# Kernel tuning notes

Hardware: AMD Instinct MI355X
Metric: run time of the kernel (lower is better)

The kernel has to match this reference:

```python
import jax, jax.numpy as jnp
import numpy as np

B, H, W = 4, 512, 512
DIM = 32          # AFNet output channels; last 3 are an RGB residual
HID = 128         # AFNet hidden width
C_IN = DIM - 3    # UNet input channels
C1, C2 = 64, 128  # UNet channel widths


def _conv(x, k, stride=1):
    # x: [B,C,H,W], k: [O,I,kh,kw]
    return jax.lax.conv_general_dilated(
        x, k, (stride, stride), 'SAME',
        dimension_numbers=('NCHW', 'OIHW', 'NCHW'))


def setup_inputs() -> dict:
    key = jax.random.key(0)
    ks = jax.random.split(key, 16)
    zbuf = jax.random.uniform(ks[0], (B, H, W, 1), jnp.float32, -0.5, 2.0)
    ray = jax.random.normal(ks[1], (B, H, W, 7), jnp.float32)
    # last ray channel is a divisor -> keep it bounded away from 0
    ray = ray.at[..., 6].set(jax.random.uniform(ks[2], (B, H, W), jnp.float32, 0.5, 1.5))
    gt = jax.random.uniform(ks[3], (B, H, W, 3), jnp.float32)
    s = 0.05
    return {
        'zbuf': zbuf, 'ray': ray, 'gt': gt, 'isTrain': 0,
        'af_w0': s * jax.random.normal(ks[4], (6, HID), jnp.float32),
        'af_b0': jnp.zeros((HID,), jnp.float32),
        'af_w1': s * jax.random.normal(ks[5], (HID, HID), jnp.float32),
        'af_b1': jnp.zeros((HID,), jnp.float32),
        'af_w2': s * jax.random.normal(ks[6], (HID, DIM), jnp.float32),
        'af_b2': jnp.zeros((DIM,), jnp.float32),
        'u_k1': s * jax.random.normal(ks[7], (C1, C_IN, 3, 3), jnp.float32),
        'u_k2': s * jax.random.normal(ks[8], (C2, C1, 3, 3), jnp.float32),
        'u_k3': s * jax.random.normal(ks[9], (C1, C2 + C1, 3, 3), jnp.float32),
        'u_k4': s * jax.random.normal(ks[10], (3, C1, 3, 3), jnp.float32),
    }


def reference(zbuf, ray, gt, isTrain, af_w0, af_b0, af_w1, af_b1, af_w2, af_b2,
              u_k1, u_k2, u_k3, u_k4):
    # Eval path (isTrain == 0): no pad / random-crop.
    pix_mask = zbuf[..., 0] > 0.0                       # [B,H,W]
    dirs = ray[..., 3:6]
    # xyz_near = origin + dir * z / ray[:, -1:]  (the gathered math, done densely)
    xyz_near = ray[..., :3] + dirs * zbuf / ray[..., 6:7]
    # AFNet: pointwise MLP on (xyz_near, dir)
    fin = jnp.concatenate([xyz_near, dirs], axis=-1)    # [B,H,W,6]
    h = jax.nn.relu(jnp.einsum('bhwi,io->bhwo', fin, af_w0) + af_b0)
    h = jax.nn.relu(jnp.einsum('bhwi,io->bhwo', h, af_w1) + af_b1)
    feat = jnp.einsum('bhwi,io->bhwo', h, af_w2) + af_b2  # [B,H,W,DIM]
    # scatter: feature_map = ones; feature_map[pix_mask] = feat
    fmap = jnp.where(pix_mask[..., None], feat, jnp.float32(1.0))
    x = jnp.transpose(fmap[..., :C_IN], (0, 3, 1, 2))     # [B,C_IN,H,W]
    rgb_res = jnp.transpose(fmap[..., C_IN:], (0, 3, 1, 2))  # [B,3,H,W]
    # UNet refine
    e1 = jax.nn.relu(_conv(x, u_k1))                      # [B,64,H,W]
    d = jax.nn.relu(_conv(e1, u_k2, stride=2))            # [B,128,H/2,W/2]
    u = jnp.repeat(jnp.repeat(d, 2, axis=2), 2, axis=3)   # nearest upsample
    m = jax.nn.relu(_conv(jnp.concatenate([u, e1], axis=1), u_k3))
    img = _conv(m, u_k4) + rgb_res                        # [B,3,H,W]
    return img
```

## Files before the change

### kernel.cpp

```cpp
#include <hip/hip_runtime.h>
#include <hip/hip_bf16.h>
#include <stdint.h>

typedef __hip_bfloat16 bf16;
typedef __attribute__((ext_vector_type(8))) short short8;
typedef __attribute__((ext_vector_type(4))) float f32x4;
typedef __attribute__((ext_vector_type(16))) float f32x16;
typedef __attribute__((ext_vector_type(8))) _Float16 half8;

__device__ __forceinline__ float bf2f(bf16 x){ return __bfloat162float(x); }
__device__ __forceinline__ bf16  f2bf(float x){ return __float2bfloat16(x); }
__device__ __forceinline__ short f2bfs(float x){ union { bf16 h; short s; } u; u.h = f2bf(x); return u.s; }
__device__ __forceinline__ float bfs2f(short s){ union { bf16 h; short t; } u; u.t = s; return bf2f(u.h); }
__device__ __forceinline__ unsigned short f2hs(float x){ union { _Float16 f; unsigned short u; } c; c.f = (_Float16)x; return c.u; }

#define WB1_R   0UL
#define WB2_R   36864UL
#define WBD_R   184320UL
#define WBE_R   446464UL
#define WB4_R   520192UL
#define WMLP_R  538624UL
#define WZERO_R 583680UL
#define W_TOTAL 587776UL
#define DT_BS   8388608UL
#define E1_BS   16777216UL
#define OUT_BS  786432UL

__global__ void prep_kernel(const float* __restrict__ uk1, const float* __restrict__ uk2,
                            const float* __restrict__ uk3, const float* __restrict__ uk4,
                            const float* __restrict__ w0, const float* __restrict__ w1,
                            const float* __restrict__ w2,
                            short* __restrict__ wb1, short* __restrict__ wb2,
                            short* __restrict__ wbD, short* __restrict__ wbE,
                            short* __restrict__ wb4,
                            unsigned short* __restrict__ wfmlp, float* __restrict__ zp){
  int gidx = blockIdx.x*256 + threadIdx.x;
  if (gidx < 18432){
    int idx = gidx;
    int j = idx & 7, lane = (idx >> 3) & 63, n = (idx >> 9) & 3, t = idx >> 11;
    int co = n*16 + (lane & 15);
    int ci = (lane >> 4)*8 + j;
    float val = (ci < 29) ? uk1[(co*29 + ci)*9 + t] : 0.f;
    wb1[idx] = f2bfs(val);
  } else if (gidx < 92160){
    int idx = gidx - 18432;
    int j    = idx & 7;
    int lane = (idx >> 3) & 63;
    int n    = (idx >> 9) & 7;
    int kt   = idx >> 12;
    int t = kt % 9, ks = kt / 9;
    int co = n*16 + (lane & 15);
    int ci = ks*32 + (lane >> 4)*8 + j;
    wb2[idx] = f2bfs(uk2[(co*64 + ci)*9 + t]);
  } else if (gidx < 223232){
    int idx = gidx - 92160;
    int j    = idx & 7;
    int lane = (idx >> 3) & 63;
    int n    = (idx >> 9) & 3;
    int kD   = (idx >> 11) & 15;
    int par  = idx >> 15;
    int pr = par >> 1, pc = par & 1;
    int jx = kD & 1, jy = (kD >> 1) & 1, ks = (kD >> 2) & 1, c = kD >> 3;
    int co = n*16 + (lane & 15);
    int ci = (c*2 + ks)*32 + (lane >> 4)*8 + j;
    int ty0, ty1, tx0, tx1;
    if (pr == 0){ ty0 = jy ? 1 : 0; ty1 = jy ? 2 : 0; }
    else        { ty0 = jy ? 2 : 0; ty1 = jy ? 2 : 1; }
    if (pc == 0){ tx0 = jx ? 1 : 0; tx1 = jx ? 2 : 0; }
    else        { tx0 = jx ? 2 : 0; tx1 = jx ? 2 : 1; }
    float val = 0.f;
    for (int ty = ty0; ty <= ty1; ++ty)
      for (int tx = tx0; tx <= tx1; ++tx)
        val += uk3[(co*192 + ci)*9 + ty*3 + tx];
    wbD[idx] = f2bfs(val);
  } else if (gidx < 260096){
    int idx = gidx - 223232;
    int j    = idx & 7;
    int lane = (idx >> 3) & 63;
    int n    = (idx >> 9) & 3;
    int chunk = idx >> 11;
    int ks2 = chunk & 1, t = chunk >> 1;
    int co = n*16 + (lane & 15);
    int ci = 128 + ks2*32 + (lane >> 4)*8 + j;
    wbE[idx] = f2bfs(uk3[(co*192 + ci)*9 + t]);
  } else if (gidx < 269312){
    int idx = gidx - 260096;
    int j = idx & 7, lane = (idx >> 3) & 63, rt = idx >> 9;
    int t = rt % 9, kc = rt / 9;
    int co = lane & 15;
    int ci = kc*32 + (lane >> 4)*8 + j;
    float val = (co < 3) ? uk4[(co*64 + ci)*9 + t] : 0.f;
    wb4[idx] = f2bfs(val);
  } else if (gidx < 291840){
    int idx = gidx - 269312;
    int j = idx & 7;
    int cl = idx >> 3;
    int lane = cl & 63;
    int chunk = cl >> 6;
    int hi5 = lane >> 5, l31 = lane & 31;
    float val;
    if (chunk < 4){
      int n = chunk;
      int k = hi5*8 + j, co = n*32 + l31;
      val = (k < 6) ? w0[k*128 + co] : 0.f;
    } else if (chunk < 36){
      int c = chunk - 4; int ks = c >> 2, n = c & 3;
      int k = ks*16 + hi5*8 + j, co = n*32 + l31;
      val = w1[k*128 + co];
    } else {
      int ks = chunk - 36;
      int k = ks*16 + hi5*8 + j, co = l31;
      val = w2[k*32 + co];
    }
    union { _Float16 f; unsigned short u; } cv; cv.f = (_Float16)val;
    wfmlp[idx] = cv.u;
  } else if (gidx < 292864){
    zp[gidx - 291840] = 0.f;
  }
}

__global__ __launch_bounds__(256,3) void mlp_mfma(
    const float* __restrict__ zbuf, const float* __restrict__ ray,
    const unsigned short* __restrict__ wf,
    bf16* __restrict__ fmap, float* __restrict__ outrgb,
    size_t fmap_bs, size_t out_bs){
  __shared__ __align__(16) unsigned short hsh[4][32][128];
  __shared__ float zsh[4][32];
  const int tid = threadIdx.x;
  const int wv = tid >> 6, lane = tid & 63, h5 = lane >> 5, l31 = lane & 31;
  const int mbase = (blockIdx.x*4 + wv)*32;
  const int bz = mbase >> 18;
  const int prel = mbase & 262143;

  const float* rp = ray + (size_t)(mbase + l31)*7;
  float z  = zbuf[mbase + l31];
  float d0 = rp[3], d1 = rp[4], d2 = rp[5];
  float inv = z / rp[6];
  half8 a1 = {};
  if (h5 == 0){
    float f[6] = { rp[0]+d0*inv, rp[1]+d1*inv, rp[2]+d2*inv, d0, d1, d2 };
    #pragma unroll
    for (int j = 0; j < 6; ++j) a1[j] = (_Float16)f[j];
    zsh[wv][l31] = z;
  }

  auto hstore = [&](int row, int col, float v){
    int g = (col >> 3) ^ (row & 7);
    hsh[wv][row][g*8 + (col & 7)] = f2hs(v);
  };
  auto hread = [&](int ks) -> half8 {
    int g = (ks*2 + h5) ^ (l31 & 7);
    return *(const half8*)&hsh[wv][l31][g*8];
  };

  f32x16 acc[4];
  #pragma unroll
  for (int n = 0; n < 4; ++n){
    half8 b = *(const half8*)&wf[(n*64 + lane)*8];
    f32x16 a = {};
    acc[n] = __builtin_amdgcn_mfma_f32_32x32x16_f16(a1, b, a, 0, 0, 0);
  }
  #pragma unroll
  for (int n = 0; n < 4; ++n)
    #pragma unroll
    for (int reg = 0; reg < 16; ++reg)
      hstore((reg&3) + 8*(reg>>2) + 4*h5, n*32 + l31, fmaxf(acc[n][reg], 0.f));

  f32x16 acc2[4];
  #pragma unroll
  for (int n = 0; n < 4; ++n) acc2[n] = (f32x16){};
  #pragma unroll
  for (int ks = 0; ks < 8; ++ks){
    half8 ah = hread(ks);
    #pragma unroll
    for (int n = 0; n < 4; ++n){
      half8 b = *(const half8*)&wf[((4 + ks*4 + n)*64 + lane)*8];
      acc2[n] = __builtin_amdgcn_mfma_f32_32x32x16_f16(ah, b, acc2[n], 0, 0, 0);
    }
  }
  #pragma unroll
  for (int n = 0; n < 4; ++n)
    #pragma unroll
    for (int reg = 0; reg < 16; ++reg)
      hstore((reg&3) + 8*(reg>>2) + 4*h5, n*32 + l31, fmaxf(acc2[n][reg], 0.f));

  f32x16 a3 = {};
  #pragma unroll
  for (int ks = 0; ks < 8; ++ks){
    half8 ah = hread(ks);
    half8 b = *(const half8*)&wf[((36 + ks)*64 + lane)*8];
    a3 = __builtin_amdgcn_mfma_f32_32x32x16_f16(ah, b, a3, 0, 0, 0);
  }

  bf16* fb = fmap + (size_t)bz*fmap_bs;
  float* ob = outrgb + (size_t)bz*out_bs;
  const int c = l31;
  #pragma unroll
  for (int g = 0; g < 4; ++g){
    const int r0 = 8*g + 4*h5;
    float vs[4];
    #pragma unroll
    for (int k = 0; k < 4; ++k){
      float zz = zsh[wv][r0 + k];
      vs[k] = (zz > 0.f) ? a3[g*4 + k] : 1.0f;
    }
    const size_t p = (size_t)(prel + r0);
    if (c < 29){
      #pragma unroll
      for (int k = 0; k < 4; ++k)
        fb[(p + k)*32 + c] = f2bf(vs[k]);
    } else {
      float4 fv = { vs[0], vs[1], vs[2], vs[3] };
      *(float4*)(&ob[((size_t)(c - 29) << 18) + p]) = fv;
      #pragma unroll
      for (int k = 0; k < 4; ++k)
        fb[(p + k)*32 + c] = f2bf(0.f);
    }
  }
}

__global__ __launch_bounds__(256,2) void conv1_mfma(
    const bf16* __restrict__ fmap32, const short8* __restrict__ wb1,
    bf16* __restrict__ e1T, const float* __restrict__ zpage,
    size_t fmap_bs, size_t e1_bs){
  __shared__ short lds[8192];
  const int tid = threadIdx.x;
  const int wv = tid >> 6, lane = tid & 63;
  const int quad = lane >> 4, l15 = lane & 15;

  const int L = blockIdx.x;
  const int cpx = gridDim.x >> 3;
  const int o = (L & 7)*cpx + (L >> 3);
  const int bx = o & 31;
  const int r2 = o >> 5;
  const int by = r2 & 63;
  const int bz = r2 >> 6;

  const bf16* fb = fmap32 + (size_t)bz*fmap_bs;
  bf16* eb = e1T + (size_t)bz*e1_bs;
  const int oy0 = by*8, ox0 = bx*16;

  for (int r = 0; r < 3; ++r){
    const int d = r*256 + tid;
    const int pairI = d >> 3, slot = d & 7;
    const int sel = slot ^ (pairI & 7);
    const int p = pairI*2 + (sel >> 2);
    const int g = sel & 3;
    const int row = p / 18, col = p - row*18;
    const int gy = oy0 - 1 + row, gx = ox0 - 1 + col;
    const bool ok = (d < 720) && ((unsigned)gy < 512u) && ((unsigned)gx < 512u);
    const void* src = ok
      ? (const void*)&fb[((size_t)((gy<<9) + gx))*32 + g*8]
      : (const void*)zpage;
    __builtin_amdgcn_global_load_lds(
      (const __attribute__((address_space(1))) void*)src,
      (__attribute__((address_space(3))) void*)&lds[d*8],
      16, 0, 0);
  }
  __syncthreads();

  f32x4 acc[2][4];
  #pragma unroll
  for (int i=0;i<2;++i)
    #pragma unroll
    for (int n=0;n<4;++n) acc[i][n] = (f32x4){0.f,0.f,0.f,0.f};

  for (int t = 0; t < 9; ++t){
    const short8* bp = wb1 + (t*4)*64 + lane;
    short8 b0 = bp[0], b1 = bp[64], b2 = bp[128], b3 = bp[192];
    const int dy = t/3, dx = t - dy*3;
    #pragma unroll
    for (int i = 0; i < 2; ++i){
      const int py = wv*2 + i + dy;
      const int px = l15 + dx;
      const int p = py*18 + px;
      const int slot = (quad + 4*(p & 1)) ^ ((p >> 1) & 7);
      short8 a = *(const short8*)&lds[((p >> 1)*8 + slot)*8];
      acc[i][0] = __builtin_amdgcn_mfma_f32_16x16x32_bf16(a, b0, acc[i][0], 0, 0, 0);
      acc[i][1] = __builtin_amdgcn_mfma_f32_16x16x32_bf16(a, b1, acc[i][1], 0, 0, 0);
      acc[i][2] = __builtin_amdgcn_mfma_f32_16x16x32_bf16(a, b2, acc[i][2], 0, 0, 0);
      acc[i][3] = __builtin_amdgcn_mfma_f32_16x16x32_bf16(a, b3, acc[i][3], 0, 0, 0);
    }
  }
  __syncthreads();

  #pragma unroll
  for (int i = 0; i < 2; ++i){
    const int rowp = wv*2 + i;
    #pragma unroll
    for (int n = 0; n < 4; ++n){
      const int gq = n*2 + (l15 >> 3);
      #pragma unroll
      for (int reg = 0; reg < 4; ++reg){
        const int px = rowp*16 + quad*4 + reg;
        const int slot = gq ^ (px & 7);
        lds[(px*8 + slot)*8 + (l15 & 7)] = f2bfs(fmaxf(acc[i][n][reg], 0.f));
      }
    }
  }
  __syncthreads();
  #pragma unroll
  for (int w = 0; w < 4; ++w){
    const int s = w*256 + tid;
    const int px = s >> 3, g8 = s & 7;
    const int slot = g8 ^ (px & 7);
    short8 v = *(const short8*)&lds[(px*8 + slot)*8];
    const int gy = oy0 + (px >> 4), gx = ox0 + (px & 15);
    *(short8*)((void*)&eb[((size_t)((gy<<9) + gx))*64 + g8*8]) = v;
  }
}

__global__ __launch_bounds__(256,2) void conv2_mfma(
    const bf16* __restrict__ e1T, const short8* __restrict__ wb2,
    bf16* __restrict__ dT, const float* __restrict__ zpage,
    size_t e1_bs, size_t dt_bs){
  __shared__ short lds[36864];
  const int tid = threadIdx.x;
  const int wv = tid >> 6, lane = tid & 63;
  const int quad = lane >> 4, l15 = lane & 15;

  const int L = blockIdx.x;
  const int cpx = gridDim.x >> 3;
  const int o = (L & 7)*cpx + (L >> 3);
  const int bx = o & 15;
  const int r2 = o >> 4;
  const int by = r2 & 31;
  const int bz = r2 >> 5;

  const bf16* eb = e1T + (size_t)bz*e1_bs;
  bf16* db = dT + (size_t)bz*dt_bs;
  const int oy0 = by*8, ox0 = bx*16;
  const int iy0 = oy0*2, ix0 = ox0*2;

  for (int r = 0; r < 18; ++r){
    const int idx = r*256 + tid;
    const int g = idx & 7, p = idx >> 3;
    const int row = p / 33, col = p - row*33;
    const int gy = iy0 + row, gx = ix0 + col;
    const int gs = g ^ ((col >> 1) & 7);
    const bool ok = (p < 561) && (gy < 512) && (gx < 512);
    const void* src = ok
      ? (const void*)&eb[((size_t)((gy<<9) + gx))*64 + gs*8]
      : (const void*)zpage;
    __builtin_amdgcn_global_load_lds(
      (const __attribute__((address_space(1))) void*)src,
      (__attribute__((address_space(3))) void*)&lds[idx*8],
      16, 0, 0);
  }
  __syncthreads();

  f32x4 acc[2][8];
  #pragma unroll
  for (int i=0;i<2;++i)
    #pragma unroll
    for (int n=0;n<8;++n) acc[i][n] = (f32x4){0.f,0.f,0.f,0.f};

  for (int ks = 0; ks < 2; ++ks){
    const int cg = ks*4 + quad;
    for (int t = 0; t < 9; ++t){
      const short8* bp = wb2 + ((ks*9 + t)*8)*64 + lane;
      short8 b0 = bp[0],   b1 = bp[64],  b2 = bp[128], b3 = bp[192];
      short8 b4 = bp[256], b5 = bp[320], b6 = bp[384], b7 = bp[448];
      const int dy = t/3, dx = t - dy*3;
      #pragma unroll
      for (int i = 0; i < 2; ++i){
        const int m = wv*2 + i;
        const int py = 2*m + dy;
        const int px = 2*l15 + dx;
        const int slot = cg ^ ((px >> 1) & 7);
        short8 a = *(const short8*)&lds[((py*33 + px)*8 + slot)*8];
        acc[i][0] = __builtin_amdgcn_mfma_f32_16x16x32_bf16(a, b0, acc[i][0], 0, 0, 0);
        acc[i][1] = __builtin_amdgcn_mfma_f32_16x16x32_bf16(a, b1, acc[i][1], 0, 0, 0);
        acc[i][2] = __builtin_amdgcn_mfma_f32_16x16x32_bf16(a, b2, acc[i][2], 0, 0, 0);
        acc[i][3] = __builtin_amdgcn_mfma_f32_16x16x32_bf16(a, b3, acc[i][3], 0, 0, 0);
        acc[i][4] = __builtin_amdgcn_mfma_f32_16x16x32_bf16(a, b4, acc[i][4], 0, 0, 0);
        acc[i][5] = __builtin_amdgcn_mfma_f32_16x16x32_bf16(a, b5, acc[i][5], 0, 0, 0);
        acc[i][6] = __builtin_amdgcn_mfma_f32_16x16x32_bf16(a, b6, acc[i][6], 0, 0, 0);
        acc[i][7] = __builtin_amdgcn_mfma_f32_16x16x32_bf16(a, b7, acc[i][7], 0, 0, 0);
      }
    }
  }
  __syncthreads();

  #pragma unroll
  for (int i = 0; i < 2; ++i){
    const int m = wv*2 + i;
    #pragma unroll
    for (int n = 0; n < 8; ++n){
      #pragma unroll
      for (int reg = 0; reg < 4; ++reg){
        const int col = quad*4 + reg;
        const int px = m*16 + col;
        const int g16 = n*2 + (l15 >> 3);
        const int slot = g16 ^ (px & 15);
        lds[(px*16 + slot)*8 + (l15 & 7)] = f2bfs(fmaxf(acc[i][n][reg], 0.f));
      }
    }
  }
  __syncthreads();
  #pragma unroll
  for (int w = 0; w < 8; ++w){
    const int s = w*256 + tid;
    const int px = s >> 4, g16 = s & 15;
    const int slot = g16 ^ (px & 15);
    short8 v = *(const short8*)&lds[(px*16 + slot)*8];
    const int gy = oy0 + (px >> 4), gx = ox0 + (px & 15);
    *(short8*)((void*)&db[((size_t)((gy<<8) + gx))*128 + g16*8]) = v;
  }
}

__global__ __launch_bounds__(256,2) void conv34_mfma(
    const bf16* __restrict__ dT, const bf16* __restrict__ e1T,
    const short8* __restrict__ wbD, const short8* __restrict__ wbE,
    const short8* __restrict__ wb4,
    float* __restrict__ out, const float* __restrict__ zpage,
    size_t dt_bs, size_t e1_bs, size_t out_bs){
  __shared__ short lds[39424];
  const int tid = threadIdx.x;
  const int wv = tid >> 6, lane = tid & 63;
  const int quad = lane >> 4, l15 = lane & 15;

  const int L = blockIdx.x;
  const int cpx = gridDim.x >> 3;
  const int o = (L & 7)*cpx + (L >> 3);
  const int bx = o % 18;
  const int rem = o / 18;
  const int by = rem & 63;
  const int bz = rem >> 6;

  const bf16* dTb = dT + (size_t)bz*dt_bs;
  const bf16* e1b = e1T + (size_t)bz*e1_bs;
  float* outb = out + (size_t)bz*out_bs;
  const int gy0 = by * 8;
  const int gx0 = bx * 30;
  const int dy0 = (gy0 >> 1) - 1;
  const int dx0 = (gx0 >> 1) - 1;
  const int rm0 = (wv >> 1) ^ 1;
  const int mx0 = (wv & 1) ^ 1;
  f32x4 acc[5][4];
  #pragma unroll
  for (int i=0;i<5;++i)
    #pragma unroll
    for (int n=0;n<4;++n) acc[i][n] = (f32x4){0.f,0.f,0.f,0.f};

  short* DB0 = lds;
  short* DB1 = lds + 6656;
  short* EB  = lds + 13312;

  auto stage_dT = [&](int c, short* db){
    #pragma unroll
    for (int r = 0; r < 4; ++r){
      const int idxb = r*256 + wv*64;
      if (idxb >= 832) continue;
      const int idx = idxb + lane;
      const int p = idx >> 3, g = idx & 7;
      const int prow = p / 17, pcol = p - prow*17;
      const int gyD = dy0 + prow, gxD = dx0 + pcol;
      const int gs = g ^ (pcol & 7);
      const bool ok = (p < 102) && ((unsigned)gyD < 256u) && ((unsigned)gxD < 256u);
      const void* src = ok
        ? (const void*)&dTb[((size_t)((gyD<<8) + gxD))*128 + c*64 + gs*8]
        : (const void*)zpage;
      __builtin_amdgcn_global_load_lds(
        (const __attribute__((address_space(1))) void*)src,
        (__attribute__((address_space(3))) void*)&db[idxb*8],
        16, 0, 0);
    }
  };

  auto stage_E = [&](short* eb){
    #pragma unroll
    for (int r = 0; r < 13; ++r){
      const int idxb = r*256 + wv*64;
      if (idxb >= 3264) continue;
      const int idx = idxb + lane;
      const int g = idx & 7, pos = idx >> 3;
      const int yy = pos / 34, xx = pos - yy*34;
      const int gy = gy0 - 2 + yy, gx = gx0 - 2 + xx;
      const int sg = g ^ ((xx >> 1) & 7);
      const bool ok = ((unsigned)gy < 512u) && ((unsigned)gx < 512u);
      const int pyc = gy & 511, pxc = gx & 511;
      const void* src = ok
        ? (const void*)&e1b[((size_t)((pyc<<9) + pxc))*64 + sg*8]
        : (const void*)zpage;
      __builtin_amdgcn_global_load_lds(
        (const __attribute__((address_space(1))) void*)src,
        (__attribute__((address_space(3))) void*)&eb[idxb*8],
        16, 0, 0);
    }
  };

  auto compute_Dc = [&](int c, const short* db){
    #pragma unroll
    for (int ks = 0; ks < 2; ++ks){
      #pragma unroll
      for (int jy = 0; jy < 2; ++jy){
        #pragma unroll
        for (int jx = 0; jx < 2; ++jx){
          const int kD = ((c*2 + ks)*2 + jy)*2 + jx;
          const short8* bp = wbD + ((size_t)(wv*16 + kD)*4)*64 + lane;
          short8 b0 = bp[0], b1 = bp[64], b2 = bp[128], b3 = bp[192];
          const int pcol = l15 + jx;
          const int g = (ks*4 + quad) ^ (pcol & 7);
          #pragma unroll
          for (int i = 0; i < 5; ++i){
            short8 a = *(const short8*)&db[((i + jy)*17 + pcol)*64 + g*8];
            acc[i][0] = __builtin_amdgcn_mfma_f32_16x16x32_bf16(a, b0, acc[i][0], 0, 0, 0);
            acc[i][1] = __builtin_amdgcn_mfma_f32_16x16x32_bf16(a, b1, acc[i][1], 0, 0, 0);
            acc[i][2] = __builtin_amdgcn_mfma_f32_16x16x32_bf16(a, b2, acc[i][2], 0, 0, 0);
            acc[i][3] = __builtin_amdgcn_mfma_f32_16x16x32_bf16(a, b3, acc[i][3], 0, 0, 0);
          }
        }
      }
    }
  };

  auto compute_E = [&](const short* eb){
    for (int t = 0; t < 9; ++t){
      const int dy = t/3, dx = t - dy*3;
      #pragma unroll
      for (int ks2 = 0; ks2 < 2; ++ks2){
        const short8* bp = wbE + ((size_t)((t*2 + ks2)*4))*64 + lane;
        short8 b0 = bp[0], b1 = bp[64], b2 = bp[128], b3 = bp[192];
        const int px = 2*l15 + mx0 + dx;
        const int g = (ks2*4 + quad) ^ ((px >> 1) & 7);
        #pragma unroll
        for (int i = 0; i < 5; ++i){
          const int row = 2*i + rm0 + dy;
          short8 a = *(const short8*)&eb[(row*34 + px)*64 + g*8];
          acc[i][0] = __builtin_amdgcn_mfma_f32_16x16x32_bf16(a, b0, acc[i][0], 0, 0, 0);
          acc[i][1] = __builtin_amdgcn_mfma_f32_16x16x32_bf16(a, b1, acc[i][1], 0, 0, 0);
          acc[i][2] = __builtin_amdgcn_mfma_f32_16x16x32_bf16(a, b2, acc[i][2], 0, 0, 0);
          acc[i][3] = __builtin_amdgcn_mfma_f32_16x16x32_bf16(a, b3, acc[i][3], 0, 0, 0);
        }
      }
    }
  };

  stage_dT(0, DB0);
  __syncthreads();

  stage_dT(1, DB1);
  __builtin_amdgcn_sched_barrier(0);
  compute_Dc(0, DB0);
  __syncthreads();

  stage_E(EB);
  __builtin_amdgcn_sched_barrier(0);
  compute_Dc(1, DB1);
  __syncthreads();

  compute_E(EB);

  __syncthreads();
  #pragma unroll
  for (int i = 0; i < 5; ++i){
    const int r = 2*i + rm0;
    const int gym = gy0 - 1 + r;
    #pragma unroll
    for (int reg = 0; reg < 4; ++reg){
      const int mxd = 2*(quad*4 + reg) + mx0;
      const int gxm = gx0 - 1 + mxd;
      const bool inim = ((unsigned)gym < 512u) && ((unsigned)gxm < 512u);
      const int key = (mxd & 7) << 3;
      #pragma unroll
      for (int n = 0; n < 4; ++n){
        float v = inim ? fmaxf(acc[i][n][reg], 0.f) : 0.f;
        int c = n*16 + l15;
        lds[(r*32 + mxd)*64 + (c ^ key)] = f2bfs(v);
      }
    }
  }
  __syncthreads();

  f32x4 a4[4];
  #pragma unroll
  for (int ii = 0; ii < 4; ++ii) a4[ii] = (f32x4){0.f,0.f,0.f,0.f};
  for (int kc = 0; kc < 2; ++kc){
    for (int t = 0; t < 9; ++t){
      short8 b = wb4[(kc*9 + t)*64 + lane];
      const int dy = t/3, dx = t - dy*3;
      #pragma unroll
      for (int ii = 0; ii < 4; ++ii){
        const int mt4 = wv*4 + ii;
        const int ly = mt4 >> 1, h = mt4 & 1;
        const int r = ly + dy;
        const int mxd = h*16 + l15 + dx;
        const int sg = (kc*4 + quad) ^ (mxd & 7);
        short8 a = *(const short8*)&lds[(r*32 + mxd)*64 + sg*8];
        a4[ii] = __builtin_amdgcn_mfma_f32_16x16x32_bf16(a, b, a4[ii], 0, 0, 0);
      }
    }
  }
  if (l15 < 3){
    #pragma unroll
    for (int ii = 0; ii < 4; ++ii){
      const int mt4 = wv*4 + ii;
      const int ly = mt4 >> 1, h = mt4 & 1;
      const int oy = gy0 + ly;
      float* op = outb + (((size_t)l15) << 18) + ((size_t)oy << 9);
      #pragma unroll
      for (int reg = 0; reg < 4; ++reg){
        const int lx = h*16 + quad*4 + reg;
        const int ox = gx0 + lx;
        if (lx < 30 && ox < 512)
          op[ox] += a4[ii][reg];
      }
    }
  }
}

static const void* find_by_size(void* const* d_in, const int* in_sizes, int n_in,
                                int want, int occurrence, int fallback_idx){
  int seen = 0;
  for (int i = 0; i < n_in; ++i){
    if (in_sizes[i] == want){
      if (seen == occurrence) return d_in[i];
      ++seen;
    }
  }
  return d_in[fallback_idx];
}

extern "C" void kernel_launch(void* const* d_in, const int* in_sizes, int n_in,
                              void* d_out, int out_size, void* d_ws, size_t ws_size,
                              hipStream_t stream) {
  const float* zbuf = (const float*)find_by_size(d_in, in_sizes, n_in, 1048576, 0, 0);
  const float* ray  = (const float*)find_by_size(d_in, in_sizes, n_in, 7340032, 0, 1);
  const float* w0   = (const float*)find_by_size(d_in, in_sizes, n_in, 768,     0, 4);
  const float* w1   = (const float*)find_by_size(d_in, in_sizes, n_in, 16384,   0, 6);
  const float* w2   = (const float*)find_by_size(d_in, in_sizes, n_in, 4096,    0, 8);
  const float* uk1  = (const float*)find_by_size(d_in, in_sizes, n_in, 16704,   0, 10);
  const float* uk2  = (const float*)find_by_size(d_in, in_sizes, n_in, 73728,   0, 11);
  const float* uk3  = (const float*)find_by_size(d_in, in_sizes, n_in, 110592,  0, 12);
  const float* uk4  = (const float*)find_by_size(d_in, in_sizes, n_in, 1728,    0, 13);

  uint8_t* ws = (uint8_t*)d_ws;
  const int batched = (ws_size >= 0xC000000UL + W_TOTAL);
  const size_t dt_off = 0;
  const size_t e1_off = batched ? 0x4000000UL : 0x1000000UL;
  const size_t w_off  = batched ? 0xC000000UL : 0x3000000UL;

  bf16* fmapB = (bf16*)(ws + dt_off);
  bf16* dTB   = (bf16*)(ws + dt_off);
  bf16* e1B   = (bf16*)(ws + e1_off);
  short* wb1  = (short*)(ws + w_off + WB1_R);
  short* wb2  = (short*)(ws + w_off + WB2_R);
  short* wbD  = (short*)(ws + w_off + WBD_R);
  short* wbE  = (short*)(ws + w_off + WBE_R);
  short* wb4  = (short*)(ws + w_off + WB4_R);
  unsigned short* wfmlp = (unsigned short*)(ws + w_off + WMLP_R);
  float* zp   = (float*)(ws + w_off + WZERO_R);
  float* outp = (float*)d_out;

  prep_kernel<<<1144, 256, 0, stream>>>(uk1, uk2, uk3, uk4, w0, w1, w2,
                                        wb1, wb2, wbD, wbE, wb4, wfmlp, zp);

  if (batched){
    mlp_mfma<<<8192, 256, 0, stream>>>(zbuf, ray, wfmlp, fmapB, outp, DT_BS, OUT_BS);
    conv1_mfma<<<8192, 256, 0, stream>>>(fmapB, (const short8*)wb1, e1B, zp, DT_BS, E1_BS);
    conv2_mfma<<<2048, 256, 0, stream>>>(e1B, (const short8*)wb2, dTB, zp, E1_BS, DT_BS);
    conv34_mfma<<<4608, 256, 0, stream>>>(dTB, e1B, (const short8*)wbD, (const short8*)wbE,
                                          (const short8*)wb4, outp, zp, DT_BS, E1_BS, OUT_BS);
  } else {
    for (int b = 0; b < 4; ++b){
      float* outb = outp + (size_t)b*OUT_BS;
      mlp_mfma<<<2048, 256, 0, stream>>>(zbuf + (size_t)b*262144,
                                         ray  + (size_t)b*262144*7,
                                         wfmlp, fmapB, outb, DT_BS, OUT_BS);
      conv1_mfma<<<2048, 256, 0, stream>>>(fmapB, (const short8*)wb1, e1B, zp, DT_BS, E1_BS);
      conv2_mfma<<<512, 256, 0, stream>>>(e1B, (const short8*)wb2, dTB, zp, E1_BS, DT_BS);
      conv34_mfma<<<1152, 256, 0, stream>>>(dTB, e1B, (const short8*)wbD, (const short8*)wbE,
                                            (const short8*)wb4, outb, zp, DT_BS, E1_BS, OUT_BS);
    }
  }
}
```

Measured before the change: 499.9 us.

## Read e1 operands directly from global memory instead of staging in LDS

The e1 skip-connection tile is no longer staged into shared memory. compute_E now issues per-lane global loads of the A operands straight from e1, which drops one barrier and shrinks the LDS allocation from about 77KB to 40KB, possibly allowing more resident blocks. In exchange, each e1 element is re-read from global/L2 up to nine times across taps, and those loads sit in the MFMA loop where latency may be exposed. The conv4 read index is also wrapped to 31 so it stays inside the smaller buffer.

```diff
diff --git a/kernel.cpp b/kernel.cpp
--- a/kernel.cpp
+++ b/kernel.cpp
@@ -415,7 +415,7 @@
     const short8* __restrict__ wb4,
     float* __restrict__ out, const float* __restrict__ zpage,
     size_t dt_bs, size_t e1_bs, size_t out_bs){
-  __shared__ short lds[39424];
+  __shared__ short lds[20480];
   const int tid = threadIdx.x;
   const int wv = tid >> 6, lane = tid & 63;
   const int quad = lane >> 4, l15 = lane & 15;
@@ -445,7 +445,6 @@
 
   short* DB0 = lds;
   short* DB1 = lds + 6656;
-  short* EB  = lds + 13312;
 
   auto stage_dT = [&](int c, short* db){
     #pragma unroll
@@ -464,28 +463,6 @@
       __builtin_amdgcn_global_load_lds(
         (const __attribute__((address_space(1))) void*)src,
         (__attribute__((address_space(3))) void*)&db[idxb*8],
-        16, 0, 0);
-    }
-  };
-
-  auto stage_E = [&](short* eb){
-    #pragma unroll
-    for (int r = 0; r < 13; ++r){
-      const int idxb = r*256 + wv*64;
-      if (idxb >= 3264) continue;
-      const int idx = idxb + lane;
-      const int g = idx & 7, pos = idx >> 3;
-      const int yy = pos / 34, xx = pos - yy*34;
-      const int gy = gy0 - 2 + yy, gx = gx0 - 2 + xx;
-      const int sg = g ^ ((xx >> 1) & 7);
-      const bool ok = ((unsigned)gy < 512u) && ((unsigned)gx < 512u);
-      const int pyc = gy & 511, pxc = gx & 511;
-      const void* src = ok
-        ? (const void*)&e1b[((size_t)((pyc<<9) + pxc))*64 + sg*8]
-        : (const void*)zpage;
-      __builtin_amdgcn_global_load_lds(
-        (const __attribute__((address_space(1))) void*)src,
-        (__attribute__((address_space(3))) void*)&eb[idxb*8],
         16, 0, 0);
     }
   };
@@ -515,7 +492,7 @@
     }
   };
 
-  auto compute_E = [&](const short* eb){
+  auto compute_E = [&](){
     for (int t = 0; t < 9; ++t){
       const int dy = t/3, dx = t - dy*3;
       #pragma unroll
@@ -523,15 +500,25 @@
         const short8* bp = wbE + ((size_t)((t*2 + ks2)*4))*64 + lane;
         short8 b0 = bp[0], b1 = bp[64], b2 = bp[128], b3 = bp[192];
         const int px = 2*l15 + mx0 + dx;
-        const int g = (ks2*4 + quad) ^ ((px >> 1) & 7);
+        const int gx = gx0 - 2 + px;
+        const int ch = ks2*4 + quad;
+        const bool okx = ((unsigned)gx < 512u);
+        short8 av[5];
         #pragma unroll
         for (int i = 0; i < 5; ++i){
-          const int row = 2*i + rm0 + dy;
-          short8 a = *(const short8*)&eb[(row*34 + px)*64 + g*8];
-          acc[i][0] = __builtin_amdgcn_mfma_f32_16x16x32_bf16(a, b0, acc[i][0], 0, 0, 0);
-          acc[i][1] = __builtin_amdgcn_mfma_f32_16x16x32_bf16(a, b1, acc[i][1], 0, 0, 0);
-          acc[i][2] = __builtin_amdgcn_mfma_f32_16x16x32_bf16(a, b2, acc[i][2], 0, 0, 0);
-          acc[i][3] = __builtin_amdgcn_mfma_f32_16x16x32_bf16(a, b3, acc[i][3], 0, 0, 0);
+          const int gy = gy0 - 2 + (2*i + rm0 + dy);
+          const bool ok = okx && ((unsigned)gy < 512u);
+          const short8* ap = ok
+            ? (const short8*)&e1b[(((size_t)gy << 9) + gx)*64 + ch*8]
+            : (const short8*)zpage;
+          av[i] = *ap;
+        }
+        #pragma unroll
+        for (int i = 0; i < 5; ++i){
+          acc[i][0] = __builtin_amdgcn_mfma_f32_16x16x32_bf16(av[i], b0, acc[i][0], 0, 0, 0);
+          acc[i][1] = __builtin_amdgcn_mfma_f32_16x16x32_bf16(av[i], b1, acc[i][1], 0, 0, 0);
+          acc[i][2] = __builtin_amdgcn_mfma_f32_16x16x32_bf16(av[i], b2, acc[i][2], 0, 0, 0);
+          acc[i][3] = __builtin_amdgcn_mfma_f32_16x16x32_bf16(av[i], b3, acc[i][3], 0, 0, 0);
         }
       }
     }
@@ -545,12 +532,8 @@
   compute_Dc(0, DB0);
   __syncthreads();
 
-  stage_E(EB);
-  __builtin_amdgcn_sched_barrier(0);
   compute_Dc(1, DB1);
-  __syncthreads();
-
-  compute_E(EB);
+  compute_E();
 
   __syncthreads();
   #pragma unroll
@@ -585,9 +568,9 @@
         const int mt4 = wv*4 + ii;
         const int ly = mt4 >> 1, h = mt4 & 1;
         const int r = ly + dy;
-        const int mxd = h*16 + l15 + dx;
-        const int sg = (kc*4 + quad) ^ (mxd & 7);
-        short8 a = *(const short8*)&lds[(r*32 + mxd)*64 + sg*8];
+        const int mxs = (h*16 + l15 + dx) & 31;
+        const int sg = (kc*4 + quad) ^ (mxs & 7);
+        short8 a = *(const short8*)&lds[(r*32 + mxs)*64 + sg*8];
         a4[ii] = __builtin_amdgcn_mfma_f32_16x16x32_bf16(a, b, a4[ii], 0, 0, 0);
       }
     }
```

Result: slower. 631.8 us (+26.4%).
